# Kernel tuning notes

Measured on AMD Instinct MI355X. Metric: run time of the kernel, lower is better.

## Reference

```python
import jax, jax.numpy as jnp
import numpy as np

N_NODES = 100000
IN_CH = 128
OUT_CH = 128
N_EDGES = 1700000


def setup_inputs() -> dict:
    key = jax.random.key(0)
    k_x, k_e, k_w = jax.random.split(key, 3)
    x = jax.random.normal(k_x, (N_NODES, IN_CH), dtype=jnp.float32)
    # edges: one self-loop per node (guarantees deg>=1 for every node),
    # remainder random
    loops = jnp.stack([jnp.arange(N_NODES, dtype=jnp.int64)] * 2)  # [2, N]
    rand = jax.random.randint(k_e, (2, N_EDGES - N_NODES), 0, N_NODES, dtype=jnp.int64)
    edge_index = jnp.concatenate([loops, rand], axis=1)  # [2, E]
    # glorot-uniform weight, zero bias (reset_parameters)
    limit = float(np.sqrt(6.0 / (IN_CH + OUT_CH)))
    weight = jax.random.uniform(k_w, (IN_CH, OUT_CH), dtype=jnp.float32,
                                minval=-limit, maxval=limit)
    bias = jnp.zeros((OUT_CH,), dtype=jnp.float32)
    return {"x": x, "edge_index": edge_index, "weight": weight, "bias": bias}


def reference(x, edge_index, weight, bias):
    row, col = edge_index[0], edge_index[1]
    # deg = bincount(row) over all N nodes
    deg = jax.ops.segment_sum(jnp.ones_like(row, dtype=jnp.float32), row,
                              num_segments=x.shape[0])
    deg_inv_sqrt = deg ** -0.5  # symmetric normalization
    norm = deg_inv_sqrt[row] * deg_inv_sqrt[col]  # [E]
    support = x @ weight  # [N, out]
    msgs = norm[:, None] * support[col]  # [E, out] gather + scale
    out = jax.ops.segment_sum(msgs, row, num_segments=x.shape[0])  # scatter-add
    return out + bias
```

## Files before the change

kernel.cpp:

```cpp
#include <hip/hip_runtime.h>
#include <hip/hip_bf16.h>


#define SCAN_B 256
#define NBLK_P 256
#define BSHIFT 9
#define NPB    512

typedef __attribute__((ext_vector_type(8))) short bf16x8;
typedef __attribute__((ext_vector_type(4))) float f32x4;

__device__ __forceinline__ uint32_t f2bf_rne(float f) {
    uint32_t u = __float_as_uint(f);
    return (u + 0x7fffu + ((u >> 16) & 1u)) >> 16;
}
__device__ __forceinline__ float bf_lo(uint32_t u) { return __uint_as_float(u << 16); }
__device__ __forceinline__ float bf_hi(uint32_t u) { return __uint_as_float(u & 0xffff0000u); }

__device__ __forceinline__ bf16x8 pack8(float4 lo, float4 hi) {
    union { bf16x8 v; ushort u[8]; } r;
    r.u[0] = (ushort)f2bf_rne(lo.x);
    r.u[1] = (ushort)f2bf_rne(lo.y);
    r.u[2] = (ushort)f2bf_rne(lo.z);
    r.u[3] = (ushort)f2bf_rne(lo.w);
    r.u[4] = (ushort)f2bf_rne(hi.x);
    r.u[5] = (ushort)f2bf_rne(hi.y);
    r.u[6] = (ushort)f2bf_rne(hi.z);
    r.u[7] = (ushort)f2bf_rne(hi.w);
    return r.v;
}

__global__ void wconv_kernel(const float* __restrict__ W, ushort* __restrict__ Wt) {
    int t = blockIdx.x * blockDim.x + threadIdx.x;
    int n = t >> 7, k = t & 127;
    Wt[n * 128 + k] = (ushort)f2bf_rne(W[k * 128 + n]);
}

__global__ __launch_bounds__(256) void mfma_gemm(const float* __restrict__ X,
                                                 const ushort* __restrict__ Wt,
                                                 uint32_t* __restrict__ S, int N) {
    const int wave = threadIdx.x >> 6;
    const int lane = threadIdx.x & 63;
    const int c16  = lane & 15;
    const int kg   = lane >> 4;
    const int row0 = blockIdx.x * 128 + wave * 32;

    int rA0 = row0 + c16;
    int rA1 = row0 + 16 + c16;
    if (rA0 >= N) rA0 = N - 1;
    if (rA1 >= N) rA1 = N - 1;

    f32x4 acc[2][8];
#pragma unroll
    for (int m = 0; m < 2; ++m)
#pragma unroll
        for (int cb = 0; cb < 8; ++cb) acc[m][cb] = (f32x4){0.f, 0.f, 0.f, 0.f};

    const float*  xa0 = X + (size_t)rA0 * 128 + kg * 8;
    const float*  xa1 = X + (size_t)rA1 * 128 + kg * 8;
    const ushort* wb  = Wt + kg * 8 + c16 * 128;

#pragma unroll
    for (int kk = 0; kk < 4; ++kk) {
        float4 a0lo = *(const float4*)(xa0 + kk * 32);
        float4 a0hi = *(const float4*)(xa0 + kk * 32 + 4);
        float4 a1lo = *(const float4*)(xa1 + kk * 32);
        float4 a1hi = *(const float4*)(xa1 + kk * 32 + 4);
        bf16x8 A0 = pack8(a0lo, a0hi);
        bf16x8 A1 = pack8(a1lo, a1hi);
#pragma unroll
        for (int cb = 0; cb < 8; ++cb) {
            bf16x8 B = *(const bf16x8*)(wb + (size_t)cb * 16 * 128 + kk * 32);
            acc[0][cb] = __builtin_amdgcn_mfma_f32_16x16x32_bf16(A0, B, acc[0][cb], 0, 0, 0);
            acc[1][cb] = __builtin_amdgcn_mfma_f32_16x16x32_bf16(A1, B, acc[1][cb], 0, 0, 0);
        }
    }
#pragma unroll
    for (int m = 0; m < 2; ++m) {
#pragma unroll
        for (int i = 0; i < 4; ++i) {
            int gr = row0 + m * 16 + kg * 4 + i;
            if (gr < N) {
#pragma unroll
                for (int cb = 0; cb < 4; ++cb) {
                    uint32_t p = f2bf_rne(acc[m][cb][i]) |
                                 (f2bf_rne(acc[m][cb + 4][i]) << 16);
                    S[(size_t)gr * 64 + cb * 16 + c16] = p;
                }
            }
        }
    }
}

__global__ __launch_bounds__(256) void p1_count(const int* __restrict__ row,
                                                int* __restrict__ cnt,
                                                int E, int chunk, int nbuck) {
    __shared__ int h[256];
    const int blk = blockIdx.x, t = threadIdx.x;
    for (int i = t; i < nbuck; i += 256) h[i] = 0;
    __syncthreads();
    int lo = blk * chunk, hi = min(E, lo + chunk);
    for (int e = lo + t; e < hi; e += 256) atomicAdd(&h[row[e] >> BSHIFT], 1);
    __syncthreads();
    for (int b = t; b < nbuck; b += 256) cnt[b * NBLK_P + blk] = h[b];
}

__global__ void scan_block_kernel(const int* __restrict__ in, int* __restrict__ outp,
                                  int* __restrict__ bsum, int M) {
    __shared__ int s[SCAN_B];
    int t = threadIdx.x;
    int g = blockIdx.x * SCAN_B + t;
    int v = (g < M) ? in[g] : 0;
    s[t] = v;
    __syncthreads();
#pragma unroll
    for (int off = 1; off < SCAN_B; off <<= 1) {
        int u = (t >= off) ? s[t - off] : 0;
        __syncthreads();
        s[t] += u;
        __syncthreads();
    }
    if (g < M) outp[g] = s[t] - v;
    if (t == SCAN_B - 1) bsum[blockIdx.x] = s[t];
}

__global__ void scan_bsum_kernel(int* __restrict__ bsum, int NB) {
    __shared__ int s[1024];
    int t = threadIdx.x;
    int v = (t < NB) ? bsum[t] : 0;
    s[t] = v;
    __syncthreads();
#pragma unroll
    for (int off = 1; off < 1024; off <<= 1) {
        int u = (t >= off) ? s[t - off] : 0;
        __syncthreads();
        s[t] += u;
        __syncthreads();
    }
    if (t < NB) bsum[t] = s[t] - v;
}

__global__ void scan_add_kernel(int* __restrict__ outp, const int* __restrict__ bsum, int M) {
    int g = blockIdx.x * blockDim.x + threadIdx.x;
    if (g < M) outp[g] += bsum[g >> 8];
}

__global__ __launch_bounds__(256) void p2_scatter(const int* __restrict__ row,
                                                  const int* __restrict__ col,
                                                  const int* __restrict__ off,
                                                  uint32_t* __restrict__ part,
                                                  int E, int chunk, int nbuck) {
    __shared__ int cur[256];
    const int blk = blockIdx.x, t = threadIdx.x;
    for (int b = t; b < nbuck; b += 256) cur[b] = off[b * NBLK_P + blk];
    __syncthreads();
    int lo = blk * chunk, hi = min(E, lo + chunk);
    for (int e = lo + t; e < hi; e += 256) {
        int r = row[e], c = col[e];
        int pos = atomicAdd(&cur[r >> BSHIFT], 1);
        part[pos] = ((uint32_t)(r & (NPB - 1)) << 17) | (uint32_t)c;
    }
}

__global__ __launch_bounds__(256) void p3_build(const uint32_t* __restrict__ part,
                                                const int* __restrict__ off,
                                                int* __restrict__ rowptr,
                                                float* __restrict__ dis,
                                                int* __restrict__ csr,
                                                int N, int E, int nbuck) {
    __shared__ int hist[NPB];
    __shared__ int lstart[NPB];
    __shared__ int s[256];
    const int b = blockIdx.x, t = threadIdx.x;
    const int base_node = b << BSHIFT;
    const int csr_base  = off[b * NBLK_P];
    const int end_b     = (b == nbuck - 1) ? E : off[(b + 1) * NBLK_P];

    for (int i = t; i < NPB; i += 256) hist[i] = 0;
    __syncthreads();
    for (int e = csr_base + t; e < end_b; e += 256)
        atomicAdd(&hist[part[e] >> 17], 1);
    __syncthreads();

    int a0 = hist[2 * t], a1 = hist[2 * t + 1];
    s[t] = a0 + a1;
    __syncthreads();
    int v = s[t];
#pragma unroll
    for (int o = 1; o < 256; o <<= 1) {
        int u = (t >= o) ? s[t - o] : 0;
        __syncthreads();
        s[t] += u;
        __syncthreads();
    }
    int ex = s[t] - v;
    lstart[2 * t]     = ex;
    lstart[2 * t + 1] = ex + a0;
    __syncthreads();

    for (int i = t; i < NPB; i += 256) {
        int node = base_node + i;
        if (node < N) {
            rowptr[node] = csr_base + lstart[i];
            dis[node]    = rsqrtf((float)hist[i]);
        }
    }
    __syncthreads();
    for (int i = t; i < NPB; i += 256) hist[i] = lstart[i];
    __syncthreads();
    for (int e = csr_base + t; e < end_b; e += 256) {
        uint32_t p = part[e];
        int pos = csr_base + atomicAdd(&hist[p >> 17], 1);
        csr[pos] = (int)(p & 0x1FFFFu);
    }
    if (b == 0 && t == 0) rowptr[N] = E;
}

__global__ __launch_bounds__(256) void gather_kernel(const int* __restrict__ csr,
                                                     const int* __restrict__ rowptr,
                                                     const float* __restrict__ dis,
                                                     const uint4* __restrict__ sup,
                                                     const float* __restrict__ bias,
                                                     float* __restrict__ out, int N) {
    int wid  = (blockIdx.x * blockDim.x + threadIdx.x) >> 6;
    int lane = threadIdx.x & 63;
    if (wid >= N) return;
    const int grp = lane >> 4;
    const int li  = lane & 15;
    int begin = rowptr[wid];
    int end   = rowptr[wid + 1];
    float dr  = dis[wid];

    float4 aL = make_float4(0.f, 0.f, 0.f, 0.f);
    float4 aH = make_float4(0.f, 0.f, 0.f, 0.f);

    for (int j = begin; j < end; j += 8) {
        int e0 = j + grp, e1 = j + 4 + grp;
        int c0 = csr[min(e0, end - 1)];
        int c1 = csr[min(e1, end - 1)];
        float n0 = (e0 < end) ? dr * dis[c0] : 0.f;
        float n1 = (e1 < end) ? dr * dis[c1] : 0.f;
        uint4 u0 = sup[(size_t)c0 * 16 + li];
        uint4 u1 = sup[(size_t)c1 * 16 + li];
        aL.x += n0 * bf_lo(u0.x) + n1 * bf_lo(u1.x);
        aL.y += n0 * bf_lo(u0.y) + n1 * bf_lo(u1.y);
        aL.z += n0 * bf_lo(u0.z) + n1 * bf_lo(u1.z);
        aL.w += n0 * bf_lo(u0.w) + n1 * bf_lo(u1.w);
        aH.x += n0 * bf_hi(u0.x) + n1 * bf_hi(u1.x);
        aH.y += n0 * bf_hi(u0.y) + n1 * bf_hi(u1.y);
        aH.z += n0 * bf_hi(u0.z) + n1 * bf_hi(u1.z);
        aH.w += n0 * bf_hi(u0.w) + n1 * bf_hi(u1.w);
    }

#pragma unroll
    for (int off = 16; off < 64; off <<= 1) {
        aL.x += __shfl_xor(aL.x, off);
        aL.y += __shfl_xor(aL.y, off);
        aL.z += __shfl_xor(aL.z, off);
        aL.w += __shfl_xor(aL.w, off);
        aH.x += __shfl_xor(aH.x, off);
        aH.y += __shfl_xor(aH.y, off);
        aH.z += __shfl_xor(aH.z, off);
        aH.w += __shfl_xor(aH.w, off);
    }

    if (grp == 0) {
        float4 bL = *(const float4*)(bias + li * 4);
        float4 bH = *(const float4*)(bias + 64 + li * 4);
        aL.x += bL.x; aL.y += bL.y; aL.z += bL.z; aL.w += bL.w;
        aH.x += bH.x; aH.y += bH.y; aH.z += bH.z; aH.w += bH.w;
        *(float4*)(out + (size_t)wid * 128 + li * 4)      = aL;
        *(float4*)(out + (size_t)wid * 128 + 64 + li * 4) = aH;
    }
}

#define GB_M 64
#define GB_KC 32
__global__ __launch_bounds__(256) void gemm_kernel(const float* __restrict__ X,
                                                   const float* __restrict__ W,
                                                   uint32_t* __restrict__ S, int N) {
    __shared__ float sXT[GB_KC][72];
    __shared__ float sW[GB_KC][128];
    const int t  = threadIdx.x;
    const int tx = t & 15;
    const int ty = t >> 4;
    const int bm = blockIdx.x * GB_M;

    float acc[4][8];
#pragma unroll
    for (int i = 0; i < 4; ++i)
#pragma unroll
        for (int j = 0; j < 8; ++j) acc[i][j] = 0.f;

    const int sr = t >> 2;
    const int sc = (t & 3) << 2;

    for (int k0 = 0; k0 < 128; k0 += GB_KC) {
#pragma unroll
        for (int h = 0; h < 2; ++h) {
            int kk = sc + h * 16;
            int gr = bm + sr;
            float4 v = make_float4(0.f, 0.f, 0.f, 0.f);
            if (gr < N) v = *(const float4*)(X + (size_t)gr * 128 + k0 + kk);
            sXT[kk + 0][sr] = v.x;
            sXT[kk + 1][sr] = v.y;
            sXT[kk + 2][sr] = v.z;
            sXT[kk + 3][sr] = v.w;
        }
#pragma unroll
        for (int h = 0; h < 4; ++h) {
            int idx = t + h * 256;
            int wk  = idx >> 5;
            int wo  = (idx & 31) << 2;
            *(float4*)&sW[wk][wo] = *(const float4*)(W + (size_t)(k0 + wk) * 128 + wo);
        }
        __syncthreads();
#pragma unroll
        for (int k = 0; k < GB_KC; ++k) {
            float4 a  = *(const float4*)&sXT[k][ty * 4];
            float4 b0 = *(const float4*)&sW[k][tx * 4];
            float4 b1 = *(const float4*)&sW[k][64 + tx * 4];
            float av[4] = {a.x, a.y, a.z, a.w};
            float bv[8] = {b0.x, b0.y, b0.z, b0.w, b1.x, b1.y, b1.z, b1.w};
#pragma unroll
            for (int i = 0; i < 4; ++i)
#pragma unroll
                for (int j = 0; j < 8; ++j) acc[i][j] += av[i] * bv[j];
        }
        __syncthreads();
    }
#pragma unroll
    for (int i = 0; i < 4; ++i) {
        int gr = bm + ty * 4 + i;
        if (gr < N) {
            uint4 q;
            q.x = f2bf_rne(acc[i][0]) | (f2bf_rne(acc[i][4]) << 16);
            q.y = f2bf_rne(acc[i][1]) | (f2bf_rne(acc[i][5]) << 16);
            q.z = f2bf_rne(acc[i][2]) | (f2bf_rne(acc[i][6]) << 16);
            q.w = f2bf_rne(acc[i][3]) | (f2bf_rne(acc[i][7]) << 16);
            *(uint4*)(S + (size_t)gr * 64 + tx * 4) = q;
        }
    }
}

__global__ void deg_i_kernel(const int* __restrict__ row, int* __restrict__ degi, int E) {
    int g = blockIdx.x * blockDim.x + threadIdx.x;
    if (g < E) atomicAdd(&degi[row[g]], 1);
}
__global__ void rsqrt_i_kernel(const int* __restrict__ degi, float* __restrict__ dis, int N) {
    int g = blockIdx.x * blockDim.x + threadIdx.x;
    if (g < N) dis[g] = rsqrtf((float)degi[g]);
}
__global__ void fill_kernel(const int* __restrict__ row, const int* __restrict__ col,
                            int* __restrict__ start, int* __restrict__ csr, int E) {
    int e = blockIdx.x * blockDim.x + threadIdx.x;
    if (e < E) {
        int pos = atomicAdd(&start[row[e]], 1);
        csr[pos] = col[e];
    }
}
__global__ void rowptr_from_start_kernel(const int* __restrict__ startv,
                                         int* __restrict__ rowptr, int N, int E) {
    int g = blockIdx.x * blockDim.x + threadIdx.x;
    if (g < N) rowptr[g] = startv[g];
    if (g == 0) rowptr[N] = E;
}

extern "C" void kernel_launch(void* const* d_in, const int* in_sizes, int n_in,
                              void* d_out, int out_size, void* d_ws, size_t ws_size,
                              hipStream_t stream) {
    const float* x    = (const float*)d_in[0];
    const int*   ei   = (const int*)d_in[1];
    const float* W    = (const float*)d_in[2];
    const float* bias = (const float*)d_in[3];
    float*       out  = (float*)d_out;

    const int N = in_sizes[0] / 128;
    const int E = in_sizes[1] / 2;
    const int* row = ei;
    const int* col = ei + E;

    const int nbuck = (N + NPB - 1) >> BSHIFT;
    const int M     = nbuck * NBLK_P;
    const int chunk = (E + NBLK_P - 1) / NBLK_P;
    const int NBm   = (M + SCAN_B - 1) / SCAN_B;

    auto al = [](size_t v) { return (v + 511) & ~(size_t)511; };
    size_t o_cnt    = 0;
    size_t o_off    = al(o_cnt + (size_t)M * 4);
    size_t o_bsum   = al(o_off + (size_t)M * 4);
    size_t o_rowptr = al(o_bsum + 4096 * 4);
    size_t o_dis    = al(o_rowptr + ((size_t)N + 1) * 4);
    size_t o_csr    = al(o_dis + (size_t)N * 4);
    size_t o_part   = al(o_csr + (size_t)E * 4);
    size_t o_wt     = al(o_part + (size_t)E * 4);
    size_t o_sup    = al(o_wt + 128 * 128 * 2);
    size_t need     = o_sup + (size_t)N * 256;

    char* ws = (char*)d_ws;

    if (ws_size >= need && nbuck <= 256 && NBm <= 1024 && N <= (1 << 17)) {
        int*      cnt    = (int*)(ws + o_cnt);
        int*      off    = (int*)(ws + o_off);
        int*      bsum   = (int*)(ws + o_bsum);
        int*      rowptr = (int*)(ws + o_rowptr);
        float*    dis    = (float*)(ws + o_dis);
        int*      csr    = (int*)(ws + o_csr);
        uint32_t* part   = (uint32_t*)(ws + o_part);
        ushort*   wt     = (ushort*)(ws + o_wt);
        uint4*    sup    = (uint4*)(ws + o_sup);

        wconv_kernel<<<64, 256, 0, stream>>>(W, wt);
        mfma_gemm<<<(N + 127) / 128, 256, 0, stream>>>(x, wt, (uint32_t*)sup, N);

        p1_count<<<NBLK_P, 256, 0, stream>>>(row, cnt, E, chunk, nbuck);
        scan_block_kernel<<<NBm, SCAN_B, 0, stream>>>(cnt, off, bsum, M);
        scan_bsum_kernel<<<1, 1024, 0, stream>>>(bsum, NBm);
        scan_add_kernel<<<NBm, SCAN_B, 0, stream>>>(off, bsum, M);
        p2_scatter<<<NBLK_P, 256, 0, stream>>>(row, col, off, part, E, chunk, nbuck);
        p3_build<<<nbuck, 256, 0, stream>>>(part, off, rowptr, dis, csr, N, E, nbuck);

        long long gthreads = (long long)N * 64;
        gather_kernel<<<(int)((gthreads + 255) / 256), 256, 0, stream>>>(
            csr, rowptr, dis, sup, bias, out, N);
    } else {
        size_t f_degi   = 0;
        size_t f_dis    = al(f_degi + (size_t)N * 4);
        size_t f_start  = al(f_dis + (size_t)N * 4);
        size_t f_rowptr = al(f_start + (size_t)N * 4);
        size_t f_bsum   = al(f_rowptr + ((size_t)N + 1) * 4);
        size_t f_csr    = al(f_bsum + 4096 * 4);
        size_t f_sup    = al(f_csr + (size_t)E * 4);

        int*      degi   = (int*)(ws + f_degi);
        float*    dis    = (float*)(ws + f_dis);
        int*      startv = (int*)(ws + f_start);
        int*      rowptr = (int*)(ws + f_rowptr);
        int*      bsum   = (int*)(ws + f_bsum);
        int*      csr    = (int*)(ws + f_csr);
        uint4*    sup    = (uint4*)(ws + f_sup);
        const int NBn = (N + SCAN_B - 1) / SCAN_B;

        hipMemsetAsync(degi, 0, (size_t)N * 4, stream);
        gemm_kernel<<<(N + GB_M - 1) / GB_M, 256, 0, stream>>>(x, W, (uint32_t*)sup, N);
        deg_i_kernel<<<(E + 255) / 256, 256, 0, stream>>>(row, degi, E);
        scan_block_kernel<<<NBn, SCAN_B, 0, stream>>>(degi, startv, bsum, N);
        scan_bsum_kernel<<<1, 1024, 0, stream>>>(bsum, NBn);
        scan_add_kernel<<<NBn, SCAN_B, 0, stream>>>(startv, bsum, N);
        rowptr_from_start_kernel<<<NBn, SCAN_B, 0, stream>>>(startv, rowptr, N, E);
        rsqrt_i_kernel<<<NBn, SCAN_B, 0, stream>>>(degi, dis, N);
        fill_kernel<<<(E + 255) / 256, 256, 0, stream>>>(row, col, startv, csr, E);
        long long gthreads = (long long)N * 64;
        gather_kernel<<<(int)((gthreads + 255) / 256), 256, 0, stream>>>(
            csr, rowptr, dis, sup, bias, out, N);
    }
}
```

Baseline: 163.7 us.

## Fold scan-add into scatter/build kernels and halve CSR bucket size

Removes the separate scan_add kernel launch by having p2_scatter and p3_build add the block-sum offset inline when reading bucket offsets. Bucket size drops from 512 to 256 nodes per bucket and the number of partition blocks doubles to 512, giving more p3_build blocks and one node per thread in the local scan. This saves a launch and a pass over the offset array, but the count array M grows fourfold (more scan work) and the per-block histograms double in size.

Result: faster. 155.8 us (-4.8%).

```diff
diff --git a/kernel.cpp b/kernel.cpp
--- a/kernel.cpp
+++ b/kernel.cpp
@@ -3,9 +3,9 @@
 
 
 #define SCAN_B 256
-#define NBLK_P 256
-#define BSHIFT 9
-#define NPB    512
+#define NBLK_P 512
+#define BSHIFT 8
+#define NPB    256
 
 typedef __attribute__((ext_vector_type(8))) short bf16x8;
 typedef __attribute__((ext_vector_type(4))) float f32x4;
@@ -95,7 +95,7 @@
 __global__ __launch_bounds__(256) void p1_count(const int* __restrict__ row,
                                                 int* __restrict__ cnt,
                                                 int E, int chunk, int nbuck) {
-    __shared__ int h[256];
+    __shared__ int h[512];
     const int blk = blockIdx.x, t = threadIdx.x;
     for (int i = t; i < nbuck; i += 256) h[i] = 0;
     __syncthreads();
@@ -140,19 +140,18 @@
     if (t < NB) bsum[t] = s[t] - v;
 }
 
-__global__ void scan_add_kernel(int* __restrict__ outp, const int* __restrict__ bsum, int M) {
-    int g = blockIdx.x * blockDim.x + threadIdx.x;
-    if (g < M) outp[g] += bsum[g >> 8];
-}
-
 __global__ __launch_bounds__(256) void p2_scatter(const int* __restrict__ row,
                                                   const int* __restrict__ col,
-                                                  const int* __restrict__ off,
+                                                  const int* __restrict__ outp,
+                                                  const int* __restrict__ bsum,
                                                   uint32_t* __restrict__ part,
                                                   int E, int chunk, int nbuck) {
-    __shared__ int cur[256];
+    __shared__ int cur[512];
     const int blk = blockIdx.x, t = threadIdx.x;
-    for (int b = t; b < nbuck; b += 256) cur[b] = off[b * NBLK_P + blk];
+    for (int b = t; b < nbuck; b += 256) {
+        int idx = b * NBLK_P + blk;
+        cur[b] = outp[idx] + bsum[idx >> 8];
+    }
     __syncthreads();
     int lo = blk * chunk, hi = min(E, lo + chunk);
     for (int e = lo + t; e < hi; e += 256) {
@@ -163,50 +162,52 @@
 }
 
 __global__ __launch_bounds__(256) void p3_build(const uint32_t* __restrict__ part,
-                                                const int* __restrict__ off,
+                                                const int* __restrict__ outp,
+                                                const int* __restrict__ bsum,
                                                 int* __restrict__ rowptr,
                                                 float* __restrict__ dis,
                                                 int* __restrict__ csr,
                                                 int N, int E, int nbuck) {
     __shared__ int hist[NPB];
     __shared__ int lstart[NPB];
-    __shared__ int s[256];
+    __shared__ int s[NPB];
     const int b = blockIdx.x, t = threadIdx.x;
     const int base_node = b << BSHIFT;
-    const int csr_base  = off[b * NBLK_P];
-    const int end_b     = (b == nbuck - 1) ? E : off[(b + 1) * NBLK_P];
-
-    for (int i = t; i < NPB; i += 256) hist[i] = 0;
+    int ib = b * NBLK_P;
+    const int csr_base = outp[ib] + bsum[ib >> 8];
+    int end_b;
+    if (b == nbuck - 1) end_b = E;
+    else {
+        int ie = (b + 1) * NBLK_P;
+        end_b = outp[ie] + bsum[ie >> 8];
+    }
+
+    hist[t] = 0;
     __syncthreads();
     for (int e = csr_base + t; e < end_b; e += 256)
         atomicAdd(&hist[part[e] >> 17], 1);
     __syncthreads();
 
-    int a0 = hist[2 * t], a1 = hist[2 * t + 1];
-    s[t] = a0 + a1;
-    __syncthreads();
-    int v = s[t];
-#pragma unroll
-    for (int o = 1; o < 256; o <<= 1) {
+    int v = hist[t];
+    s[t] = v;
+    __syncthreads();
+#pragma unroll
+    for (int o = 1; o < NPB; o <<= 1) {
         int u = (t >= o) ? s[t - o] : 0;
         __syncthreads();
         s[t] += u;
         __syncthreads();
     }
-    int ex = s[t] - v;
-    lstart[2 * t]     = ex;
-    lstart[2 * t + 1] = ex + a0;
-    __syncthreads();
-
-    for (int i = t; i < NPB; i += 256) {
-        int node = base_node + i;
-        if (node < N) {
-            rowptr[node] = csr_base + lstart[i];
-            dis[node]    = rsqrtf((float)hist[i]);
-        }
-    }
-    __syncthreads();
-    for (int i = t; i < NPB; i += 256) hist[i] = lstart[i];
+    lstart[t] = s[t] - v;
+    __syncthreads();
+
+    int node = base_node + t;
+    if (node < N) {
+        rowptr[node] = csr_base + lstart[t];
+        dis[node]    = rsqrtf((float)hist[t]);
+    }
+    __syncthreads();
+    hist[t] = lstart[t];
     __syncthreads();
     for (int e = csr_base + t; e < end_b; e += 256) {
         uint32_t p = part[e];
@@ -229,6 +230,7 @@
     const int li  = lane & 15;
     int begin = rowptr[wid];
     int end   = rowptr[wid + 1];
+    int endm1 = end - 1;
     float dr  = dis[wid];
 
     float4 aL = make_float4(0.f, 0.f, 0.f, 0.f);
@@ -236,8 +238,8 @@
 
     for (int j = begin; j < end; j += 8) {
         int e0 = j + grp, e1 = j + 4 + grp;
-        int c0 = csr[min(e0, end - 1)];
-        int c1 = csr[min(e1, end - 1)];
+        int c0 = csr[min(e0, endm1)];
+        int c1 = csr[min(e1, endm1)];
         float n0 = (e0 < end) ? dr * dis[c0] : 0.f;
         float n1 = (e1 < end) ? dr * dis[c1] : 0.f;
         uint4 u0 = sup[(size_t)c0 * 16 + li];
@@ -274,6 +276,10 @@
     }
 }
 
+__global__ void scan_add_kernel(int* __restrict__ outp, const int* __restrict__ bsum, int M) {
+    int g = blockIdx.x * blockDim.x + threadIdx.x;
+    if (g < M) outp[g] += bsum[g >> 8];
+}
 #define GB_M 64
 #define GB_KC 32
 __global__ __launch_bounds__(256) void gemm_kernel(const float* __restrict__ X,
@@ -342,7 +348,6 @@
         }
     }
 }
-
 __global__ void deg_i_kernel(const int* __restrict__ row, int* __restrict__ degi, int E) {
     int g = blockIdx.x * blockDim.x + threadIdx.x;
     if (g < E) atomicAdd(&degi[row[g]], 1);
@@ -399,7 +404,7 @@
 
     char* ws = (char*)d_ws;
 
-    if (ws_size >= need && nbuck <= 256 && NBm <= 1024 && N <= (1 << 17)) {
+    if (ws_size >= need && nbuck <= 512 && NBm <= 1024 && N <= (1 << 17)) {
         int*      cnt    = (int*)(ws + o_cnt);
         int*      off    = (int*)(ws + o_off);
         int*      bsum   = (int*)(ws + o_bsum);
@@ -416,9 +421,8 @@
         p1_count<<<NBLK_P, 256, 0, stream>>>(row, cnt, E, chunk, nbuck);
         scan_block_kernel<<<NBm, SCAN_B, 0, stream>>>(cnt, off, bsum, M);
         scan_bsum_kernel<<<1, 1024, 0, stream>>>(bsum, NBm);
-        scan_add_kernel<<<NBm, SCAN_B, 0, stream>>>(off, bsum, M);
-        p2_scatter<<<NBLK_P, 256, 0, stream>>>(row, col, off, part, E, chunk, nbuck);
-        p3_build<<<nbuck, 256, 0, stream>>>(part, off, rowptr, dis, csr, N, E, nbuck);
+        p2_scatter<<<NBLK_P, 256, 0, stream>>>(row, col, off, bsum, part, E, chunk, nbuck);
+        p3_build<<<nbuck, 256, 0, stream>>>(part, off, bsum, rowptr, dis, csr, N, E, nbuck);
 
         long long gthreads = (long long)N * 64;
         gather_kernel<<<(int)((gthreads + 255) / 256), 256, 0, stream>>>(
```
